# Kernel optimization log

Measured on AMD Instinct MI355X. Metric: run time of the kernel, lower is better.

## Reference

```python
import jax, jax.numpy as jnp
import numpy as np

B, C, H, W = 8, 64, 32, 32
NEG = 256
TEMP = 2.0
FACTOR = 0.8
EPS = 1e-8


def setup_inputs() -> dict:
    key = jax.random.key(0)
    k1, k2, k3, k4 = jax.random.split(key, 4)
    views_1 = jax.random.normal(k1, (B, C, H, W), dtype=jnp.float32)
    views_2 = jax.random.normal(k2, (B, C, H, W), dtype=jnp.float32)
    img = jax.random.uniform(k3, (1, 3, H, W), dtype=jnp.float32)
    neg_idx = jax.random.randint(k4, (B, 2, H * W, NEG), 0, H, dtype=jnp.int32)
    return {"views_1": views_1, "views_2": views_2, "img": img, "neg_idx": neg_idx}


def _forward(views_1, views_2, img, neg_idx):
    hw = H * W
    height = jnp.arange(hw) // W
    width = jnp.arange(hw) % W
    coords = jnp.stack([height, width]).astype(jnp.float32)  # [2, hw]
    img0 = img[0]  # [3, H, W]; original uses img[0] for EVERY batch element
    euc_norm = jnp.sqrt(jnp.asarray((H - 1) ** 2 + (W - 1) ** 2, jnp.float32))
    sqrt3 = jnp.sqrt(jnp.asarray(3.0, jnp.float32))

    center = img0[:, height, width]  # [3, hw]

    def per_sample(z1, z2, nidx):
        # nidx: [2, hw, neg]
        nf = nidx.astype(jnp.float32)
        # torch.norm with no dim => scalar Frobenius norm over [2, neg] per pixel
        d = coords[:, :, None] - nf  # [2, hw, neg]
        euc = jnp.sqrt(jnp.sum(d * d, axis=(0, 2))) / euc_norm  # [hw]
        negs = img0[:, nidx[0], nidx[1]]  # [3, hw, neg]
        rd = center[:, :, None] - negs
        rgb = jnp.sqrt(jnp.sum(rd * rd, axis=(0, 2))) / sqrt3  # [hw]
        weight = euc * FACTOR + rgb * (1.0 - FACTOR)  # [hw], constant across neg

        z1v = z1.reshape(C, hw)  # [c, hw]
        pn = z2[:, nidx[0], nidx[1]]  # [c, hw, neg]
        dot = jnp.einsum('cp,cpn->pn', z1v, pn)  # [hw, neg]
        z1sq = jnp.sum(z1v * z1v, axis=0)  # [hw]
        z1n = jnp.sqrt(z1sq)
        pnn = jnp.sqrt(jnp.sum(pn * pn, axis=0))  # [hw, neg]
        cos = dot / jnp.maximum(z1n[:, None] * pnn, EPS)  # [hw, neg]
        cos0 = z1sq / jnp.maximum(z1sq, EPS)  # [hw] (self-similarity ~ 1)

        sim_neg = jnp.minimum(jnp.abs(cos * weight[:, None]), 1.0)  # [hw, neg]
        sim0 = jnp.minimum(jnp.abs(cos0), 1.0)  # [hw]
        sim = jnp.concatenate(
            [jnp.mean(sim0)[None], jnp.mean(sim_neg, axis=0) / TEMP]
        )  # [neg+1]

        # BCELoss with target = [1, 0, ..., 0]; torch clamps log terms at -100
        logp = jnp.maximum(jnp.log(sim[0]), -100.0)
        log1m = jnp.maximum(jnp.log1p(-sim[1:]), -100.0)
        bce = -(logp + jnp.sum(log1m)) / (NEG + 1)
        return bce, sim

    bce, sims = jax.vmap(per_sample)(views_1, views_2, neg_idx)
    loss = jnp.mean(bce)
    sim_all = jnp.sum(sims, axis=0)
    return (loss, sim_all[0] / B, jnp.sum(sim_all[1:]) / NEG * TEMP / B)


def reference(views_1, views_2, img, neg_idx):
    return _forward(views_1, views_2, img, neg_idx)
```

## Files before the change

kernel.cpp:

```cpp
#include <hip/hip_runtime.h>
#include <math.h>

#define BB 8
#define CC 64
#define HH 32
#define WW 32
#define HW 1024
#define NEGN 256
#define TEMP 2.0f
#define FACTOR 0.8f
#define EPSF 1e-8f
#define PT 8
#define RING 8


__global__ __launch_bounds__(256, 4) void contrastive_fused(
    const float* __restrict__ z1,
    const float* __restrict__ z2,
    const float* __restrict__ img,
    const int*   __restrict__ nidx,
    float* __restrict__ simPart,
    float* __restrict__ sim0Part)
{
    __shared__ float As_s[CC * PT];
    __shared__ float Dt_s[PT * HW];
    __shared__ float z1n_s[PT];
    __shared__ float z1sq_s[PT];

    const int t   = threadIdx.x;
    const int blk = blockIdx.x;
    const int b   = blk >> 7;
    const int p0  = (blk & 127) * PT;

    const int lane32 = t & 31;
    const int pp_b   = t >> 5;
    const int p_b    = p0 + pp_b;

    const size_t nbase = ((size_t)(b * 2) * HW + p_b) * NEGN;
    const int2* __restrict__ nr = reinterpret_cast<const int2*>(nidx + nbase);
    const int2* __restrict__ nc =
        reinterpret_cast<const int2*>(nidx + nbase + (size_t)HW * NEGN);
    int2 rrv[4], ccv[4];
    #pragma unroll
    for (int j = 0; j < 4; ++j) {
        rrv[j] = nr[lane32 + 32 * j];
        ccv[j] = nc[lane32 + 32 * j];
    }

    for (int i = t; i < CC * PT; i += 256) {
        const int c = i >> 3, pp = i & 7;
        As_s[i] = z1[((size_t)(b * CC + c)) * HW + p0 + pp];
    }
    float* imgs_l = Dt_s;
    {
        const float4* __restrict__ imgf4 = reinterpret_cast<const float4*>(img);
        float4* imgs4 = reinterpret_cast<float4*>(imgs_l);
        #pragma unroll
        for (int j = 0; j < 3; ++j) imgs4[t + 256 * j] = imgf4[t + 256 * j];
    }

    const float4* __restrict__ z2f4 =
        reinterpret_cast<const float4*>(z2 + (size_t)b * CC * HW);
    float4 pf[RING];
    #pragma unroll
    for (int i = 0; i < RING; ++i) pf[i] = z2f4[i * (HW / 4) + t];

    __syncthreads();

    {
        const int pp = t & 7;
        float s = 0.f;
        #pragma unroll
        for (int c = 0; c < CC; ++c) { const float v = As_s[c * PT + pp]; s += v * v; }
        if (t < PT) { z1sq_s[t] = s; z1n_s[t] = sqrtf(s); }
    }

    const float cen0 = imgs_l[p_b], cen1 = imgs_l[HW + p_b], cen2 = imgs_l[2 * HW + p_b];
    const float hp = (float)(p_b >> 5), wp = (float)(p_b & 31);

    int q[8];
    #pragma unroll
    for (int j = 0; j < 4; ++j) {
        q[2 * j]     = rrv[j].x * WW + ccv[j].x;
        q[2 * j + 1] = rrv[j].y * WW + ccv[j].y;
    }
    float g0[8], g1[8], g2[8];
    #pragma unroll
    for (int e = 0; e < 8; ++e) {
        g0[e] = imgs_l[q[e]];
        g1[e] = imgs_l[HW + q[e]];
        g2[e] = imgs_l[2 * HW + q[e]];
    }
    float se = 0.f, sr = 0.f;
    #pragma unroll
    for (int j = 0; j < 4; ++j) {
        {
            const float dh = hp - (float)rrv[j].x, dw = wp - (float)ccv[j].x;
            se += dh * dh + dw * dw;
            const float d0 = cen0 - g0[2 * j];
            const float d1 = cen1 - g1[2 * j];
            const float d2 = cen2 - g2[2 * j];
            sr += d0 * d0 + d1 * d1 + d2 * d2;
        }
        {
            const float dh = hp - (float)rrv[j].y, dw = wp - (float)ccv[j].y;
            se += dh * dh + dw * dw;
            const float d0 = cen0 - g0[2 * j + 1];
            const float d1 = cen1 - g1[2 * j + 1];
            const float d2 = cen2 - g2[2 * j + 1];
            sr += d0 * d0 + d1 * d1 + d2 * d2;
        }
    }
    #pragma unroll
    for (int off = 16; off; off >>= 1) {
        se += __shfl_xor(se, off);
        sr += __shfl_xor(sr, off);
    }
    const float euc_norm = sqrtf((float)((HH - 1) * (HH - 1) + (WW - 1) * (WW - 1)));
    const float weight = sqrtf(se) / euc_norm * FACTOR +
                         sqrtf(sr) / sqrtf(3.0f) * (1.0f - FACTOR);

    __syncthreads();

    if (t == 0) {
        float s0 = 0.f;
        #pragma unroll
        for (int pp = 0; pp < PT; ++pp)
            s0 += fminf(fabsf(z1sq_s[pp] / fmaxf(z1sq_s[pp], EPSF)), 1.0f);
        sim0Part[blk] = s0;
    }

    float4 acc[PT];
    #pragma unroll
    for (int pp = 0; pp < PT; ++pp) acc[pp] = make_float4(0.f, 0.f, 0.f, 0.f);
    float4 sq = make_float4(0.f, 0.f, 0.f, 0.f);

#define GEMM_STEP(kk, bv)                                                      \
    {                                                                          \
        sq.x = fmaf((bv).x, (bv).x, sq.x);                                     \
        sq.y = fmaf((bv).y, (bv).y, sq.y);                                     \
        sq.z = fmaf((bv).z, (bv).z, sq.z);                                     \
        sq.w = fmaf((bv).w, (bv).w, sq.w);                                     \
        const float4 a03 = reinterpret_cast<const float4*>(As_s)[(kk) * 2];    \
        const float4 a47 = reinterpret_cast<const float4*>(As_s)[(kk) * 2 + 1];\
        const float av[8] = {a03.x, a03.y, a03.z, a03.w,                       \
                             a47.x, a47.y, a47.z, a47.w};                      \
        _Pragma("unroll")                                                      \
        for (int pp = 0; pp < PT; ++pp) {                                      \
            acc[pp].x = fmaf(av[pp], (bv).x, acc[pp].x);                       \
            acc[pp].y = fmaf(av[pp], (bv).y, acc[pp].y);                       \
            acc[pp].z = fmaf(av[pp], (bv).z, acc[pp].z);                       \
            acc[pp].w = fmaf(av[pp], (bv).w, acc[pp].w);                       \
        }                                                                      \
    }

    #pragma unroll 8
    for (int k = 0; k < CC - RING; ++k) {
        const float4 bv = pf[k & (RING - 1)];
        pf[k & (RING - 1)] = z2f4[(k + RING) * (HW / 4) + t];
        GEMM_STEP(k, bv);
    }
    #pragma unroll
    for (int k = CC - RING; k < CC; ++k) {
        const float4 bv = pf[k & (RING - 1)];
        GEMM_STEP(k, bv);
    }
#undef GEMM_STEP

    float z1nv[PT];
    #pragma unroll
    for (int pp = 0; pp < PT; ++pp) z1nv[pp] = z1n_s[pp];
    const float4 pnn = make_float4(sqrtf(sq.x), sqrtf(sq.y),
                                   sqrtf(sq.z), sqrtf(sq.w));
    float4* Dt4 = reinterpret_cast<float4*>(Dt_s);
    #pragma unroll
    for (int pp = 0; pp < PT; ++pp) {
        float4 cv;
        cv.x = acc[pp].x / fmaxf(z1nv[pp] * pnn.x, EPSF);
        cv.y = acc[pp].y / fmaxf(z1nv[pp] * pnn.y, EPSF);
        cv.z = acc[pp].z / fmaxf(z1nv[pp] * pnn.z, EPSF);
        cv.w = acc[pp].w / fmaxf(z1nv[pp] * pnn.w, EPSF);
        Dt4[pp * (HW / 4) + t] = cv;
    }
    __syncthreads();

    float cg[8];
    #pragma unroll
    for (int e = 0; e < 8; ++e) cg[e] = Dt_s[pp_b * HW + q[e]];

    float2 sv[4];
    #pragma unroll
    for (int j = 0; j < 4; ++j) {
        sv[j].x = fminf(fabsf(cg[2 * j]     * weight), 1.0f);
        sv[j].y = fminf(fabsf(cg[2 * j + 1] * weight), 1.0f);
    }

    __syncthreads();
    float2* simpart2 = reinterpret_cast<float2*>(Dt_s);
    #pragma unroll
    for (int j = 0; j < 4; ++j)
        simpart2[pp_b * (NEGN / 2) + lane32 + 32 * j] = sv[j];
    __syncthreads();

    float s = 0.f;
    #pragma unroll
    for (int pp = 0; pp < PT; ++pp) s += Dt_s[pp * NEGN + t];
    simPart[(size_t)blk * NEGN + t] = s;
}

__global__ __launch_bounds__(256) void reduce_out(
    const float* __restrict__ simPart,
    const float* __restrict__ sim0Part,
    float* __restrict__ out)
{
    const int b = blockIdx.x;
    const int t = threadIdx.x;

    float a = 0.f;
    #pragma unroll 8
    for (int pblk = 0; pblk < 128; ++pblk)
        a += simPart[((size_t)(b * 128 + pblk)) * NEGN + t];

    const float s = a * (1.0f / HW) * (1.0f / TEMP);
    float ssum = s;
    float lsum = fmaxf(log1pf(-s), -100.0f);

    __shared__ float rs[4], rl[4];
    __shared__ float s0sh;
    #pragma unroll
    for (int off = 32; off; off >>= 1) {
        ssum += __shfl_down(ssum, off);
        lsum += __shfl_down(lsum, off);
    }
    if ((t & 63) == 0) { rs[t >> 6] = ssum; rl[t >> 6] = lsum; }

    if (t < 64) {
        float v = sim0Part[b * 128 + t] + sim0Part[b * 128 + 64 + t];
        #pragma unroll
        for (int off = 32; off; off >>= 1) v += __shfl_xor(v, off);
        if (t == 0) s0sh = v * (1.0f / HW);
    }
    __syncthreads();

    if (t == 0) {
        const float S = rs[0] + rs[1] + rs[2] + rs[3];
        const float L = rl[0] + rl[1] + rl[2] + rl[3];
        const float s0 = s0sh;
        const float logp = fmaxf(logf(s0), -100.0f);
        atomicAdd(out + 0, -(logp + L) / ((float)(NEGN + 1) * (float)BB));
        atomicAdd(out + 1, s0 / (float)BB);
        atomicAdd(out + 2, S / (float)NEGN * TEMP / (float)BB);
    }
}

extern "C" void kernel_launch(void* const* d_in, const int* in_sizes, int n_in,
                              void* d_out, int out_size, void* d_ws, size_t ws_size,
                              hipStream_t stream) {
    const float* v1   = (const float*)d_in[0];
    const float* v2   = (const float*)d_in[1];
    const float* img  = (const float*)d_in[2];
    const int*   nidx = (const int*)  d_in[3];

    float* simPart  = (float*)d_ws;
    float* sim0Part = simPart + 1024 * NEGN;

    contrastive_fused<<<BB * (HW / PT), 256, 0, stream>>>(
        v1, v2, img, nidx, simPart, sim0Part);
    reduce_out<<<BB, 256, 0, stream>>>(simPart, sim0Part, (float*)d_out);
}
```

Measured before the change: 102.8 us.

## Split fused kernel into weight/index phase and GEMM-similarity phase

Splits the single fused kernel into two. The first reads the negative indices and image, computes per-pixel weights, and writes compact 16-bit flattened indices to workspace. The second does the z1·z2 GEMM and gathers cosine values through those precomputed indices. The aim is to cut register and shared-memory pressure in the GEMM kernel and shrink its index traffic, at the cost of an extra launch and a workspace round trip.

Measured after the change: 103.3 us. Within noise of the previous version (+0.5%).

```diff
diff --git a/kernel.cpp b/kernel.cpp
--- a/kernel.cpp
+++ b/kernel.cpp
@@ -14,18 +14,13 @@
 #define RING 8
 
 
-__global__ __launch_bounds__(256, 4) void contrastive_fused(
-    const float* __restrict__ z1,
-    const float* __restrict__ z2,
+__global__ __launch_bounds__(256) void weight_phase(
     const float* __restrict__ img,
     const int*   __restrict__ nidx,
-    float* __restrict__ simPart,
-    float* __restrict__ sim0Part)
+    ushort2* __restrict__ qp,
+    float* __restrict__ weight_g)
 {
-    __shared__ float As_s[CC * PT];
-    __shared__ float Dt_s[PT * HW];
-    __shared__ float z1n_s[PT];
-    __shared__ float z1sq_s[PT];
+    __shared__ float imgs_l[3 * HW];
 
     const int t   = threadIdx.x;
     const int blk = blockIdx.x;
@@ -47,33 +42,13 @@
         ccv[j] = nc[lane32 + 32 * j];
     }
 
-    for (int i = t; i < CC * PT; i += 256) {
-        const int c = i >> 3, pp = i & 7;
-        As_s[i] = z1[((size_t)(b * CC + c)) * HW + p0 + pp];
-    }
-    float* imgs_l = Dt_s;
     {
         const float4* __restrict__ imgf4 = reinterpret_cast<const float4*>(img);
         float4* imgs4 = reinterpret_cast<float4*>(imgs_l);
         #pragma unroll
         for (int j = 0; j < 3; ++j) imgs4[t + 256 * j] = imgf4[t + 256 * j];
     }
-
-    const float4* __restrict__ z2f4 =
-        reinterpret_cast<const float4*>(z2 + (size_t)b * CC * HW);
-    float4 pf[RING];
-    #pragma unroll
-    for (int i = 0; i < RING; ++i) pf[i] = z2f4[i * (HW / 4) + t];
-
-    __syncthreads();
-
-    {
-        const int pp = t & 7;
-        float s = 0.f;
-        #pragma unroll
-        for (int c = 0; c < CC; ++c) { const float v = As_s[c * PT + pp]; s += v * v; }
-        if (t < PT) { z1sq_s[t] = s; z1n_s[t] = sqrtf(s); }
-    }
+    __syncthreads();
 
     const float cen0 = imgs_l[p_b], cen1 = imgs_l[HW + p_b], cen2 = imgs_l[2 * HW + p_b];
     const float hp = (float)(p_b >> 5), wp = (float)(p_b & 31);
@@ -120,6 +95,54 @@
     const float weight = sqrtf(se) / euc_norm * FACTOR +
                          sqrtf(sr) / sqrtf(3.0f) * (1.0f - FACTOR);
 
+    ushort2* qrow = qp + (size_t)blk * 1024;
+    #pragma unroll
+    for (int j = 0; j < 4; ++j)
+        qrow[pp_b * 128 + lane32 + 32 * j] =
+            make_ushort2((unsigned short)q[2 * j], (unsigned short)q[2 * j + 1]);
+    if (lane32 == 0) weight_g[blk * 8 + pp_b] = weight;
+}
+
+__global__ __launch_bounds__(256, 4) void gemm_sim(
+    const float* __restrict__ z1,
+    const float* __restrict__ z2,
+    const ushort2* __restrict__ qp,
+    const float* __restrict__ weight_g,
+    float* __restrict__ simPart,
+    float* __restrict__ sim0Part)
+{
+    __shared__ float As_s[CC * PT];
+    __shared__ float Dt_s[PT * HW];
+    __shared__ float z1n_s[PT];
+    __shared__ float z1sq_s[PT];
+
+    const int t   = threadIdx.x;
+    const int blk = blockIdx.x;
+    const int b   = blk >> 7;
+    const int p0  = (blk & 127) * PT;
+
+    const int lane32 = t & 31;
+    const int pp_b   = t >> 5;
+
+    for (int i = t; i < CC * PT; i += 256) {
+        const int c = i >> 3, pp = i & 7;
+        As_s[i] = z1[((size_t)(b * CC + c)) * HW + p0 + pp];
+    }
+    const float4* __restrict__ z2f4 =
+        reinterpret_cast<const float4*>(z2 + (size_t)b * CC * HW);
+    float4 pf[RING];
+    #pragma unroll
+    for (int i = 0; i < RING; ++i) pf[i] = z2f4[i * (HW / 4) + t];
+
+    __syncthreads();
+
+    {
+        const int pp = t & 7;
+        float s = 0.f;
+        #pragma unroll
+        for (int c = 0; c < CC; ++c) { const float v = As_s[c * PT + pp]; s += v * v; }
+        if (t < PT) { z1sq_s[t] = s; z1n_s[t] = sqrtf(s); }
+    }
     __syncthreads();
 
     if (t == 0) {
@@ -182,12 +205,20 @@
         cv.w = acc[pp].w / fmaxf(z1nv[pp] * pnn.w, EPSF);
         Dt4[pp * (HW / 4) + t] = cv;
     }
+
+    const ushort2* qrow = qp + (size_t)blk * 1024;
+    ushort2 qv[4];
+    #pragma unroll
+    for (int j = 0; j < 4; ++j) qv[j] = qrow[pp_b * 128 + lane32 + 32 * j];
+    const float weight = weight_g[blk * 8 + pp_b];
     __syncthreads();
 
     float cg[8];
     #pragma unroll
-    for (int e = 0; e < 8; ++e) cg[e] = Dt_s[pp_b * HW + q[e]];
-
+    for (int j = 0; j < 4; ++j) {
+        cg[2 * j]     = Dt_s[pp_b * HW + qv[j].x];
+        cg[2 * j + 1] = Dt_s[pp_b * HW + qv[j].y];
+    }
     float2 sv[4];
     #pragma unroll
     for (int j = 0; j < 4; ++j) {
@@ -261,10 +292,13 @@
     const float* img  = (const float*)d_in[2];
     const int*   nidx = (const int*)  d_in[3];
 
-    float* simPart  = (float*)d_ws;
-    float* sim0Part = simPart + 1024 * NEGN;
-
-    contrastive_fused<<<BB * (HW / PT), 256, 0, stream>>>(
-        v1, v2, img, nidx, simPart, sim0Part);
+    float*   simPart  = (float*)d_ws;
+    float*   sim0Part = simPart + 1024 * NEGN;
+    float*   weight_g = sim0Part + 1024;
+    ushort2* qp       = (ushort2*)(weight_g + 1024 * 8);
+
+    weight_phase<<<BB * (HW / PT), 256, 0, stream>>>(img, nidx, qp, weight_g);
+    gemm_sim<<<BB * (HW / PT), 256, 0, stream>>>(
+        v1, v2, qp, weight_g, simPart, sim0Part);
     reduce_out<<<BB, 256, 0, stream>>>(simPart, sim0Part, (float*)d_out);
 }
```

## Split into prep and bf16 MFMA GEMM kernels with packed indices

Applied to the files above, without the earlier changes.

Adds a prep kernel that computes per-pixel weights, packs gather indices to ushort2, computes z1/z2 norms, and transposes z1/z2 into bf16 row-major buffers. A second kernel computes the 16x1024 dot-product tile per block with 16x16x32 bf16 MFMA instructions instead of fp32 FMA loops, then gathers and reduces as before. This moves the dense dot products onto the matrix cores and halves operand bytes. In exchange it adds an extra kernel launch, workspace round-trips, and bf16 rounding of the cosine inputs, which lowers precision. Norms stay in fp32.

New measurement: 91.35 us. 1.12x faster.

```diff
diff --git a/kernel.cpp b/kernel.cpp
--- a/kernel.cpp
+++ b/kernel.cpp
@@ -10,33 +10,50 @@
 #define TEMP 2.0f
 #define FACTOR 0.8f
 #define EPSF 1e-8f
-#define PT 8
-#define RING 8
-
-
-__global__ __launch_bounds__(256, 4) void contrastive_fused(
+
+typedef short bf16x8 __attribute__((ext_vector_type(8)));
+typedef float f32x4  __attribute__((ext_vector_type(4)));
+
+__device__ inline unsigned short f2bf(float f) {
+    unsigned u = __float_as_uint(f);
+    u += 0x7FFFu + ((u >> 16) & 1u);
+    return (unsigned short)(u >> 16);
+}
+
+
+__global__ __launch_bounds__(256) void prep(
     const float* __restrict__ z1,
     const float* __restrict__ z2,
     const float* __restrict__ img,
     const int*   __restrict__ nidx,
-    float* __restrict__ simPart,
+    ushort2* __restrict__ qp,
+    float* __restrict__ weight_g,
+    unsigned short* __restrict__ z1t,
+    unsigned short* __restrict__ z2t,
+    float* __restrict__ z1n_ws,
+    float* __restrict__ normq_ws,
     float* __restrict__ sim0Part)
 {
-    __shared__ float As_s[CC * PT];
-    __shared__ float Dt_s[PT * HW];
-    __shared__ float z1n_s[PT];
-    __shared__ float z1sq_s[PT];
+    __shared__ float imgs_l[3 * HW];
+    __shared__ float ctile[64 * 16];
+    __shared__ float csq[16];
 
     const int t   = threadIdx.x;
     const int blk = blockIdx.x;
-    const int b   = blk >> 7;
-    const int p0  = (blk & 127) * PT;
-
+
+    const int b_w  = blk >> 7;
+    const int p0_8 = (blk & 127) * 8;
     const int lane32 = t & 31;
-    const int pp_b   = t >> 5;
-    const int p_b    = p0 + pp_b;
-
-    const size_t nbase = ((size_t)(b * 2) * HW + p_b) * NEGN;
+    const int pp_w   = t >> 5;
+    const int p_w    = p0_8 + pp_w;
+
+    const bool isZ1 = (blk < 512);
+    const int cvt   = isZ1 ? blk : blk - 512;
+    const int b_c   = cvt >> 6;
+    const int p0c   = (cvt & 63) * 16;
+    const float* __restrict__ src = isZ1 ? z1 : z2;
+
+    const size_t nbase = ((size_t)(b_w * 2) * HW + p_w) * NEGN;
     const int2* __restrict__ nr = reinterpret_cast<const int2*>(nidx + nbase);
     const int2* __restrict__ nc =
         reinterpret_cast<const int2*>(nidx + nbase + (size_t)HW * NEGN);
@@ -47,164 +64,189 @@
         ccv[j] = nc[lane32 + 32 * j];
     }
 
-    for (int i = t; i < CC * PT; i += 256) {
-        const int c = i >> 3, pp = i & 7;
-        As_s[i] = z1[((size_t)(b * CC + c)) * HW + p0 + pp];
-    }
-    float* imgs_l = Dt_s;
     {
         const float4* __restrict__ imgf4 = reinterpret_cast<const float4*>(img);
         float4* imgs4 = reinterpret_cast<float4*>(imgs_l);
         #pragma unroll
         for (int j = 0; j < 3; ++j) imgs4[t + 256 * j] = imgf4[t + 256 * j];
     }
-
-    const float4* __restrict__ z2f4 =
-        reinterpret_cast<const float4*>(z2 + (size_t)b * CC * HW);
-    float4 pf[RING];
-    #pragma unroll
-    for (int i = 0; i < RING; ++i) pf[i] = z2f4[i * (HW / 4) + t];
-
-    __syncthreads();
-
     {
-        const int pp = t & 7;
+        #pragma unroll
+        for (int i = 0; i < 4; ++i) {
+            const int idx = t + 256 * i;
+            const int c = idx >> 4, row = idx & 15;
+            ctile[idx] = src[((size_t)(b_c * CC + c)) * HW + p0c + row];
+        }
+    }
+    __syncthreads();
+
+    {
+        const float cen0 = imgs_l[p_w], cen1 = imgs_l[HW + p_w], cen2 = imgs_l[2 * HW + p_w];
+        const float hp = (float)(p_w >> 5), wp = (float)(p_w & 31);
+
+        int q[8];
+        #pragma unroll
+        for (int j = 0; j < 4; ++j) {
+            q[2 * j]     = rrv[j].x * WW + ccv[j].x;
+            q[2 * j + 1] = rrv[j].y * WW + ccv[j].y;
+        }
+        float g0[8], g1[8], g2[8];
+        #pragma unroll
+        for (int e = 0; e < 8; ++e) {
+            g0[e] = imgs_l[q[e]];
+            g1[e] = imgs_l[HW + q[e]];
+            g2[e] = imgs_l[2 * HW + q[e]];
+        }
+        float se = 0.f, sr = 0.f;
+        #pragma unroll
+        for (int j = 0; j < 4; ++j) {
+            {
+                const float dh = hp - (float)rrv[j].x, dw = wp - (float)ccv[j].x;
+                se += dh * dh + dw * dw;
+                const float d0 = cen0 - g0[2 * j];
+                const float d1 = cen1 - g1[2 * j];
+                const float d2 = cen2 - g2[2 * j];
+                sr += d0 * d0 + d1 * d1 + d2 * d2;
+            }
+            {
+                const float dh = hp - (float)rrv[j].y, dw = wp - (float)ccv[j].y;
+                se += dh * dh + dw * dw;
+                const float d0 = cen0 - g0[2 * j + 1];
+                const float d1 = cen1 - g1[2 * j + 1];
+                const float d2 = cen2 - g2[2 * j + 1];
+                sr += d0 * d0 + d1 * d1 + d2 * d2;
+            }
+        }
+        #pragma unroll
+        for (int off = 16; off; off >>= 1) {
+            se += __shfl_xor(se, off);
+            sr += __shfl_xor(sr, off);
+        }
+        const float euc_norm = sqrtf((float)((HH - 1) * (HH - 1) + (WW - 1) * (WW - 1)));
+        const float weight = sqrtf(se) / euc_norm * FACTOR +
+                             sqrtf(sr) / sqrtf(3.0f) * (1.0f - FACTOR);
+
+        ushort2* qrow = qp + (size_t)(b_w * 1024 + p0_8) * 128;
+        #pragma unroll
+        for (int j = 0; j < 4; ++j)
+            qrow[pp_w * 128 + lane32 + 32 * j] =
+                make_ushort2((unsigned short)q[2 * j], (unsigned short)q[2 * j + 1]);
+        if (lane32 == 0) weight_g[b_w * 1024 + p_w] = weight;
+    }
+
+    if (t < 16) {
         float s = 0.f;
         #pragma unroll
-        for (int c = 0; c < CC; ++c) { const float v = As_s[c * PT + pp]; s += v * v; }
-        if (t < PT) { z1sq_s[t] = s; z1n_s[t] = sqrtf(s); }
-    }
-
-    const float cen0 = imgs_l[p_b], cen1 = imgs_l[HW + p_b], cen2 = imgs_l[2 * HW + p_b];
-    const float hp = (float)(p_b >> 5), wp = (float)(p_b & 31);
-
-    int q[8];
-    #pragma unroll
-    for (int j = 0; j < 4; ++j) {
-        q[2 * j]     = rrv[j].x * WW + ccv[j].x;
-        q[2 * j + 1] = rrv[j].y * WW + ccv[j].y;
-    }
-    float g0[8], g1[8], g2[8];
-    #pragma unroll
-    for (int e = 0; e < 8; ++e) {
-        g0[e] = imgs_l[q[e]];
-        g1[e] = imgs_l[HW + q[e]];
-        g2[e] = imgs_l[2 * HW + q[e]];
-    }
-    float se = 0.f, sr = 0.f;
-    #pragma unroll
-    for (int j = 0; j < 4; ++j) {
-        {
-            const float dh = hp - (float)rrv[j].x, dw = wp - (float)ccv[j].x;
-            se += dh * dh + dw * dw;
-            const float d0 = cen0 - g0[2 * j];
-            const float d1 = cen1 - g1[2 * j];
-            const float d2 = cen2 - g2[2 * j];
-            sr += d0 * d0 + d1 * d1 + d2 * d2;
-        }
-        {
-            const float dh = hp - (float)rrv[j].y, dw = wp - (float)ccv[j].y;
-            se += dh * dh + dw * dw;
-            const float d0 = cen0 - g0[2 * j + 1];
-            const float d1 = cen1 - g1[2 * j + 1];
-            const float d2 = cen2 - g2[2 * j + 1];
-            sr += d0 * d0 + d1 * d1 + d2 * d2;
-        }
-    }
-    #pragma unroll
-    for (int off = 16; off; off >>= 1) {
-        se += __shfl_xor(se, off);
-        sr += __shfl_xor(sr, off);
-    }
-    const float euc_norm = sqrtf((float)((HH - 1) * (HH - 1) + (WW - 1) * (WW - 1)));
-    const float weight = sqrtf(se) / euc_norm * FACTOR +
-                         sqrtf(sr) / sqrtf(3.0f) * (1.0f - FACTOR);
-
-    __syncthreads();
-
-    if (t == 0) {
+        for (int c = 0; c < CC; ++c) { const float v = ctile[c * 16 + t]; s += v * v; }
+        if (isZ1) {
+            z1n_ws[b_c * 1024 + p0c + t] = sqrtf(s);
+            csq[t] = fminf(fabsf(s / fmaxf(s, EPSF)), 1.0f);
+        } else {
+            normq_ws[b_c * 1024 + p0c + t] = sqrtf(s);
+        }
+    }
+    __syncthreads();
+    if (isZ1 && t == 0) {
         float s0 = 0.f;
         #pragma unroll
-        for (int pp = 0; pp < PT; ++pp)
-            s0 += fminf(fabsf(z1sq_s[pp] / fmaxf(z1sq_s[pp], EPSF)), 1.0f);
-        sim0Part[blk] = s0;
-    }
-
-    float4 acc[PT];
-    #pragma unroll
-    for (int pp = 0; pp < PT; ++pp) acc[pp] = make_float4(0.f, 0.f, 0.f, 0.f);
-    float4 sq = make_float4(0.f, 0.f, 0.f, 0.f);
-
-#define GEMM_STEP(kk, bv)                                                      \
-    {                                                                          \
-        sq.x = fmaf((bv).x, (bv).x, sq.x);                                     \
-        sq.y = fmaf((bv).y, (bv).y, sq.y);                                     \
-        sq.z = fmaf((bv).z, (bv).z, sq.z);                                     \
-        sq.w = fmaf((bv).w, (bv).w, sq.w);                                     \
-        const float4 a03 = reinterpret_cast<const float4*>(As_s)[(kk) * 2];    \
-        const float4 a47 = reinterpret_cast<const float4*>(As_s)[(kk) * 2 + 1];\
-        const float av[8] = {a03.x, a03.y, a03.z, a03.w,                       \
-                             a47.x, a47.y, a47.z, a47.w};                      \
-        _Pragma("unroll")                                                      \
-        for (int pp = 0; pp < PT; ++pp) {                                      \
-            acc[pp].x = fmaf(av[pp], (bv).x, acc[pp].x);                       \
-            acc[pp].y = fmaf(av[pp], (bv).y, acc[pp].y);                       \
-            acc[pp].z = fmaf(av[pp], (bv).z, acc[pp].z);                       \
-            acc[pp].w = fmaf(av[pp], (bv).w, acc[pp].w);                       \
-        }                                                                      \
-    }
-
-    #pragma unroll 8
-    for (int k = 0; k < CC - RING; ++k) {
-        const float4 bv = pf[k & (RING - 1)];
-        pf[k & (RING - 1)] = z2f4[(k + RING) * (HW / 4) + t];
-        GEMM_STEP(k, bv);
-    }
-    #pragma unroll
-    for (int k = CC - RING; k < CC; ++k) {
-        const float4 bv = pf[k & (RING - 1)];
-        GEMM_STEP(k, bv);
-    }
-#undef GEMM_STEP
-
-    float z1nv[PT];
-    #pragma unroll
-    for (int pp = 0; pp < PT; ++pp) z1nv[pp] = z1n_s[pp];
-    const float4 pnn = make_float4(sqrtf(sq.x), sqrtf(sq.y),
-                                   sqrtf(sq.z), sqrtf(sq.w));
-    float4* Dt4 = reinterpret_cast<float4*>(Dt_s);
-    #pragma unroll
-    for (int pp = 0; pp < PT; ++pp) {
-        float4 cv;
-        cv.x = acc[pp].x / fmaxf(z1nv[pp] * pnn.x, EPSF);
-        cv.y = acc[pp].y / fmaxf(z1nv[pp] * pnn.y, EPSF);
-        cv.z = acc[pp].z / fmaxf(z1nv[pp] * pnn.z, EPSF);
-        cv.w = acc[pp].w / fmaxf(z1nv[pp] * pnn.w, EPSF);
-        Dt4[pp * (HW / 4) + t] = cv;
-    }
-    __syncthreads();
-
-    float cg[8];
-    #pragma unroll
-    for (int e = 0; e < 8; ++e) cg[e] = Dt_s[pp_b * HW + q[e]];
-
-    float2 sv[4];
-    #pragma unroll
-    for (int j = 0; j < 4; ++j) {
-        sv[j].x = fminf(fabsf(cg[2 * j]     * weight), 1.0f);
-        sv[j].y = fminf(fabsf(cg[2 * j + 1] * weight), 1.0f);
-    }
-
-    __syncthreads();
+        for (int i = 0; i < 16; ++i) s0 += csq[i];
+        sim0Part[cvt] = s0;
+    }
+
+    {
+        unsigned short* dst =
+            (isZ1 ? z1t : z2t) + ((size_t)(b_c * 1024) + p0c) * 64;
+        ushort4 pk;
+        const int o = 4 * t;
+        pk.x = f2bf(ctile[((o + 0) & 63) * 16 + ((o + 0) >> 6)]);
+        pk.y = f2bf(ctile[((o + 1) & 63) * 16 + ((o + 1) >> 6)]);
+        pk.z = f2bf(ctile[((o + 2) & 63) * 16 + ((o + 2) >> 6)]);
+        pk.w = f2bf(ctile[((o + 3) & 63) * 16 + ((o + 3) >> 6)]);
+        *reinterpret_cast<ushort4*>(dst + o) = pk;
+    }
+}
+
+__global__ __launch_bounds__(256, 2) void gemm_mfma(
+    const unsigned short* __restrict__ z1t,
+    const unsigned short* __restrict__ z2t,
+    const float* __restrict__ z1n_ws,
+    const float* __restrict__ normq_ws,
+    const ushort2* __restrict__ qp,
+    const float* __restrict__ weight_g,
+    float* __restrict__ simPart)
+{
+    __shared__ float Dt_s[16 * HW];
+    __shared__ float nq_s[HW];
+    __shared__ float z1n_s[16];
+
+    const int t    = threadIdx.x;
+    const int blk  = blockIdx.x;
+    const int b    = blk >> 6;
+    const int p0   = (blk & 63) * 16;
+    const int wave = t >> 6;
+    const int lane = t & 63;
+    const int ln15 = lane & 15;
+    const int lg   = lane >> 4;
+
+    reinterpret_cast<float4*>(nq_s)[t] =
+        reinterpret_cast<const float4*>(normq_ws + b * 1024)[t];
+    if (t < 16) z1n_s[t] = z1n_ws[b * 1024 + p0 + t];
+
+    const unsigned short* arow =
+        z1t + ((size_t)(b * 1024) + p0 + ln15) * 64 + lg * 8;
+    const bf16x8 a0 = *reinterpret_cast<const bf16x8*>(arow);
+    const bf16x8 a1 = *reinterpret_cast<const bf16x8*>(arow + 32);
+
+    __syncthreads();
+
+    const int qw = wave * 256;
+    #pragma unroll 4
+    for (int tile = 0; tile < 16; ++tile) {
+        const int q0 = qw + tile * 16;
+        const unsigned short* brow =
+            z2t + ((size_t)(b * 1024) + q0 + ln15) * 64 + lg * 8;
+        const bf16x8 b0 = *reinterpret_cast<const bf16x8*>(brow);
+        const bf16x8 b1 = *reinterpret_cast<const bf16x8*>(brow + 32);
+        f32x4 acc = {0.f, 0.f, 0.f, 0.f};
+        acc = __builtin_amdgcn_mfma_f32_16x16x32_bf16(a0, b0, acc, 0, 0, 0);
+        acc = __builtin_amdgcn_mfma_f32_16x16x32_bf16(a1, b1, acc, 0, 0, 0);
+
+        const float pn = nq_s[q0 + ln15];
+        #pragma unroll
+        for (int i = 0; i < 4; ++i) {
+            const int row = lg * 4 + i;
+            Dt_s[row * HW + q0 + ln15] = acc[i] / fmaxf(z1n_s[row] * pn, EPSF);
+        }
+    }
+
+    const int p_b = t >> 4;
+    const int tn  = t & 15;
+    const ushort2* qrow = qp + (size_t)(b * 1024 + p0 + p_b) * 128;
+    ushort2 qv[8];
+    #pragma unroll
+    for (int j = 0; j < 8; ++j) qv[j] = qrow[tn + 16 * j];
+    const float weight = weight_g[b * 1024 + p0 + p_b];
+    __syncthreads();
+
+    float2 sv[8];
+    #pragma unroll
+    for (int j = 0; j < 8; ++j) {
+        const float c0 = Dt_s[p_b * HW + qv[j].x];
+        const float c1 = Dt_s[p_b * HW + qv[j].y];
+        sv[j].x = fminf(fabsf(c0 * weight), 1.0f);
+        sv[j].y = fminf(fabsf(c1 * weight), 1.0f);
+    }
+    __syncthreads();
+
     float2* simpart2 = reinterpret_cast<float2*>(Dt_s);
     #pragma unroll
-    for (int j = 0; j < 4; ++j)
-        simpart2[pp_b * (NEGN / 2) + lane32 + 32 * j] = sv[j];
+    for (int j = 0; j < 8; ++j)
+        simpart2[p_b * (NEGN / 2) + tn + 16 * j] = sv[j];
     __syncthreads();
 
     float s = 0.f;
     #pragma unroll
-    for (int pp = 0; pp < PT; ++pp) s += Dt_s[pp * NEGN + t];
+    for (int pp = 0; pp < 16; ++pp) s += Dt_s[pp * NEGN + t];
     simPart[(size_t)blk * NEGN + t] = s;
 }
 
@@ -218,8 +260,8 @@
 
     float a = 0.f;
     #pragma unroll 8
-    for (int pblk = 0; pblk < 128; ++pblk)
-        a += simPart[((size_t)(b * 128 + pblk)) * NEGN + t];
+    for (int pblk = 0; pblk < 64; ++pblk)
+        a += simPart[((size_t)(b * 64 + pblk)) * NEGN + t];
 
     const float s = a * (1.0f / HW) * (1.0f / TEMP);
     float ssum = s;
@@ -235,7 +277,7 @@
     if ((t & 63) == 0) { rs[t >> 6] = ssum; rl[t >> 6] = lsum; }
 
     if (t < 64) {
-        float v = sim0Part[b * 128 + t] + sim0Part[b * 128 + 64 + t];
+        float v = sim0Part[b * 64 + t];
         #pragma unroll
         for (int off = 32; off; off >>= 1) v += __shfl_xor(v, off);
         if (t == 0) s0sh = v * (1.0f / HW);
@@ -261,10 +303,18 @@
     const float* img  = (const float*)d_in[2];
     const int*   nidx = (const int*)  d_in[3];
 
-    float* simPart  = (float*)d_ws;
-    float* sim0Part = simPart + 1024 * NEGN;
-
-    contrastive_fused<<<BB * (HW / PT), 256, 0, stream>>>(
-        v1, v2, img, nidx, simPart, sim0Part);
+    float*   simPart  = (float*)d_ws;
+    float*   sim0Part = simPart + 512 * NEGN;
+    float*   weight_g = sim0Part + 512;
+    float*   z1n_ws   = weight_g + 8192;
+    float*   normq_ws = z1n_ws + 8192;
+    ushort2* qp       = (ushort2*)(normq_ws + 8192);
+    unsigned short* z1t = (unsigned short*)(qp + 1048576);
+    unsigned short* z2t = z1t + 8 * 1024 * 64;
+
+    prep<<<1024, 256, 0, stream>>>(v1, v2, img, nidx, qp, weight_g,
+                                   z1t, z2t, z1n_ws, normq_ws, sim0Part);
+    gemm_mfma<<<512, 256, 0, stream>>>(z1t, z2t, z1n_ws, normq_ws,
+                                       qp, weight_g, simPart);
     reduce_out<<<BB, 256, 0, stream>>>(simPart, sim0Part, (float*)d_out);
 }
```
